# Performance work log

Measured on AMD Instinct MI355X. Metric: run time of the kernel, lower is better.

## Reference

```python
import jax, jax.numpy as jnp
import numpy as np

B, L, N = 256, 512, 50000

def setup_inputs() -> dict:
    key = jax.random.key(0)
    k1, k2 = jax.random.split(key)
    loc_seq = jax.random.randint(k1, (B, L), 0, N, dtype=jnp.int64) if jax.config.jax_enable_x64 else jax.random.randint(k1, (B, L), 0, N, dtype=jnp.int32)
    mask = jax.random.randint(k2, (B, L), 0, 2, dtype=jnp.int32)
    return {
        "loc_seq": loc_seq,
        "mask": mask,
        "recency_weight": jnp.float32(0.85),
        "frequency_weight": jnp.float32(1.5),
        "num_locations": N,
    }

def reference(loc_seq, mask, recency_weight, frequency_weight, num_locations):
    Bsz, Lseq = loc_seq.shape
    valid = mask.astype(jnp.float32)                       # (B, L)
    # position_from_end = L - 1 - t, so recency factor per timestep t
    pos_from_end = jnp.arange(Lseq - 1, -1, -1, dtype=jnp.float32)  # (L,)
    rec_vals = jnp.power(recency_weight, pos_from_end)[None, :] * valid  # (B, L)
    b_idx = jnp.arange(Bsz)[:, None]                       # (B, 1) broadcast with (B, L)
    # running scatter-max starting from zeros == single scatter-max of all timesteps
    recency_scores = jnp.zeros((Bsz, num_locations), jnp.float32).at[b_idx, loc_seq].max(rec_vals)
    # scatter-add of validity counts
    frequency_counts = jnp.zeros((Bsz, num_locations), jnp.float32).at[b_idx, loc_seq].add(valid)
    max_freq = jnp.maximum(frequency_counts.max(axis=1, keepdims=True), 1.0)
    frequency_normalized = frequency_counts / max_freq
    return recency_scores + frequency_weight * frequency_normalized
```

## Files before the change

kernel.cpp:

```cpp
#include <hip/hip_runtime.h>
#include <hip/hip_bf16.h>


constexpr int kB = 256;
constexpr int kL = 512;
constexpr int kN = 50000;

__global__ __launch_bounds__(kL, 1) void loc_hist_enc_kernel(
    const int* __restrict__ loc_seq,
    const int* __restrict__ mask,
    const float* __restrict__ rw_p,
    const float* __restrict__ fw_p,
    float* __restrict__ out)
{
    const int b = blockIdx.x;
    const int t = threadIdx.x;

    __shared__ int   s_pk[kL];
    __shared__ float s_red[kL / 64];
    __shared__ float s_mf;

    const float rw = rw_p[0];
    const float fw = fw_p[0];

    const int loc = loc_seq[b * kL + t];
    const int v   = mask[b * kL + t];
    s_pk[t] = loc | (v << 16);
    __syncthreads();

    float4* __restrict__ orow = reinterpret_cast<float4*>(out + (size_t)b * kN);
    const float4 z4 = make_float4(0.f, 0.f, 0.f, 0.f);
    #pragma unroll 5
    for (int i = t; i < kN / 4; i += kL) orow[i] = z4;

    const int target = loc | (1 << 16);
    int freq = 0;
    int first = 0x7fffffff;
    int last  = -1;
    #pragma unroll 8
    for (int j = 0; j < kL; ++j) {
        const int  pj = s_pk[j];
        const bool eq = (pj == target);
        freq += eq ? 1 : 0;
        first = min(first, eq ? j : 0x7fffffff);
        last  = eq ? j : last;
    }
    const float f = (float)freq;

    float mf = f;
    #pragma unroll
    for (int off = 32; off >= 1; off >>= 1)
        mf = fmaxf(mf, __shfl_xor(mf, off));
    if ((t & 63) == 0) s_red[t >> 6] = mf;
    __syncthreads();
    if (t == 0) {
        float m = 1.0f;
        #pragma unroll
        for (int w = 0; w < kL / 64; ++w) m = fmaxf(m, s_red[w]);
        s_mf = m;
    }
    __syncthreads();

    if (v && first == t) {
        const float rec = fmaxf(powf(rw, (float)(kL - 1 - last)),
                                powf(rw, (float)(kL - 1 - first)));
        out[(size_t)b * kN + loc] = rec + fw * (f / s_mf);
    }
}

extern "C" void kernel_launch(void* const* d_in, const int* in_sizes, int n_in,
                              void* d_out, int out_size, void* d_ws, size_t ws_size,
                              hipStream_t stream) {
    const int*   loc_seq = (const int*)d_in[0];
    const int*   mask    = (const int*)d_in[1];
    const float* rw      = (const float*)d_in[2];
    const float* fw      = (const float*)d_in[3];
    float* out = (float*)d_out;

    loc_hist_enc_kernel<<<kB, kL, 0, stream>>>(loc_seq, mask, rw, fw, out);
}
```

Baseline: 91.74 us.

## Replace quadratic per-thread scan with shared-memory hash table histogram

Swaps the O(L^2) loop, in which every thread scans all 512 packed entries to count matches, for a shared-memory open-addressing hash table. Slots are claimed with atomicCAS, then atomic add/min/max record count and first/last timestep. Recency powers are precomputed into a shared table, and each hash slot writes one output. This removes the quadratic LDS scan but adds atomic contention and probe loops, and the zeroing store loop still dominates memory traffic.

Result: faster. 79.67 us (-13.2%).

```diff
diff --git a/kernel.cpp b/kernel.cpp
--- a/kernel.cpp
+++ b/kernel.cpp
@@ -5,6 +5,11 @@
 constexpr int kB = 256;
 constexpr int kL = 512;
 constexpr int kN = 50000;
+constexpr int kH = 1024;
+
+__device__ __forceinline__ int hash_loc(int loc) {
+    return (int)(((unsigned)loc * 2654435761u) >> 16) & (kH - 1);
+}
 
 __global__ __launch_bounds__(kL, 1) void loc_hist_enc_kernel(
     const int* __restrict__ loc_seq,
@@ -16,38 +21,50 @@
     const int b = blockIdx.x;
     const int t = threadIdx.x;
 
-    __shared__ int   s_pk[kL];
+    __shared__ int   h_key[kH];
+    __shared__ int   h_cnt[kH];
+    __shared__ int   h_tmin[kH];
+    __shared__ int   h_tmax[kH];
+    __shared__ float s_pw[kL];
     __shared__ float s_red[kL / 64];
     __shared__ float s_mf;
 
     const float rw = rw_p[0];
     const float fw = fw_p[0];
 
+    #pragma unroll
+    for (int s = t; s < kH; s += kL) {
+        h_key[s]  = -1;
+        h_cnt[s]  = 0;
+        h_tmin[s] = 0x7fffffff;
+        h_tmax[s] = -1;
+    }
+    s_pw[t] = powf(rw, (float)t);
+
     const int loc = loc_seq[b * kL + t];
     const int v   = mask[b * kL + t];
-    s_pk[t] = loc | (v << 16);
-    __syncthreads();
 
     float4* __restrict__ orow = reinterpret_cast<float4*>(out + (size_t)b * kN);
     const float4 z4 = make_float4(0.f, 0.f, 0.f, 0.f);
     #pragma unroll 5
     for (int i = t; i < kN / 4; i += kL) orow[i] = z4;
 
-    const int target = loc | (1 << 16);
-    int freq = 0;
-    int first = 0x7fffffff;
-    int last  = -1;
-    #pragma unroll 8
-    for (int j = 0; j < kL; ++j) {
-        const int  pj = s_pk[j];
-        const bool eq = (pj == target);
-        freq += eq ? 1 : 0;
-        first = min(first, eq ? j : 0x7fffffff);
-        last  = eq ? j : last;
+    __syncthreads();
+
+    if (v) {
+        int s = hash_loc(loc);
+        while (true) {
+            const int k = atomicCAS(&h_key[s], -1, loc);
+            if (k == -1 || k == loc) break;
+            s = (s + 1) & (kH - 1);
+        }
+        atomicAdd(&h_cnt[s], 1);
+        atomicMin(&h_tmin[s], t);
+        atomicMax(&h_tmax[s], t);
     }
-    const float f = (float)freq;
+    __syncthreads();
 
-    float mf = f;
+    float mf = fmaxf((float)h_cnt[t], (float)h_cnt[t + kL]);
     #pragma unroll
     for (int off = 32; off >= 1; off >>= 1)
         mf = fmaxf(mf, __shfl_xor(mf, off));
@@ -61,10 +78,15 @@
     }
     __syncthreads();
 
-    if (v && first == t) {
-        const float rec = fmaxf(powf(rw, (float)(kL - 1 - last)),
-                                powf(rw, (float)(kL - 1 - first)));
-        out[(size_t)b * kN + loc] = rec + fw * (f / s_mf);
+    const float inv_mf = s_mf;
+    #pragma unroll
+    for (int s = t; s < kH; s += kL) {
+        const int key = h_key[s];
+        if (key >= 0) {
+            const float rec = fmaxf(s_pw[kL - 1 - h_tmax[s]],
+                                    s_pw[kL - 1 - h_tmin[s]]);
+            out[(size_t)b * kN + key] = rec + fw * ((float)h_cnt[s] / inv_mf);
+        }
     }
 }
 
```
